# Kernel optimization log

Hardware: AMD Instinct MI355X
Metric: run time of the kernel (lower is better)

## Reference

```python
import jax, jax.numpy as jnp
import numpy as np

USER_NUM = 100000
ITEM_NUM = 100000
EMB = 128
N_USERS = 65536
N_BEH = 2097152
N_GROUPS = 2048


def setup_inputs() -> dict:
    key = jax.random.key(0)
    ks = jax.random.split(key, 7)
    user_ids = jax.random.randint(ks[0], (N_USERS,), 0, USER_NUM, dtype=jnp.int32)
    user_group_ids = jnp.sort(jax.random.randint(ks[1], (N_USERS,), 0, N_GROUPS, dtype=jnp.int32))
    behavior_item_ids = jax.random.randint(ks[2], (N_BEH,), 0, ITEM_NUM, dtype=jnp.int32)
    behavior_counts = jax.random.uniform(ks[3], (N_BEH,), dtype=jnp.float32)
    behavior_user_ids = jnp.sort(jax.random.randint(ks[4], (N_BEH,), 0, N_USERS, dtype=jnp.int32))
    user_table = jax.random.normal(ks[5], (USER_NUM, EMB), dtype=jnp.float32)
    item_table = jax.random.normal(ks[6], (ITEM_NUM, EMB), dtype=jnp.float32)
    return {
        "user_ids": user_ids,
        "user_group_ids": user_group_ids,
        "behavior_item_ids": behavior_item_ids,
        "behavior_counts": behavior_counts,
        "behavior_user_ids": behavior_user_ids,
        "user_table": user_table,
        "item_table": item_table,
        "num_groups": N_GROUPS,
    }


def reference(user_ids, user_group_ids, behavior_item_ids, behavior_counts,
              behavior_user_ids, user_table, item_table, num_groups):
    n_users = user_ids.shape[0]
    # weighted bag-of-items per user: sum_j item_emb[b_id] * count  -> [n_users, EMB]
    beh_emb = item_table[behavior_item_ids] * behavior_counts[:, None]
    per_user_beh = jax.ops.segment_sum(beh_emb, behavior_user_ids, num_segments=n_users)
    # user embedding with padding_idx=0 (id 0 -> zero vector)
    ue = user_table[user_ids] * (user_ids != 0).astype(user_table.dtype)[:, None]
    per_user = per_user_beh * ue  # personalized behavior embedding
    # pooling == 'sum' over users within each group -> [num_groups, EMB]
    group_embedding = jax.ops.segment_sum(per_user, user_group_ids, num_segments=num_groups)
    return group_embedding
```

## Files before the change

kernel.cpp:

```cpp
#include <hip/hip_runtime.h>
#include <hip/hip_fp16.h>

#define EMB 128

__global__ __launch_bounds__(256) void convert_kernel(
    const float* __restrict__ src, __half* __restrict__ dst, int n8)
{
    int t = blockIdx.x * 256 + threadIdx.x;
    if (t >= n8) return;
    const float4* s = (const float4*)src + (size_t)t * 2;
    float4 f0 = s[0];
    float4 f1 = s[1];
    union { __half h[8]; uint4 u; } pk;
    pk.h[0] = __float2half_rn(f0.x); pk.h[1] = __float2half_rn(f0.y);
    pk.h[2] = __float2half_rn(f0.z); pk.h[3] = __float2half_rn(f0.w);
    pk.h[4] = __float2half_rn(f1.x); pk.h[5] = __float2half_rn(f1.y);
    pk.h[6] = __float2half_rn(f1.z); pk.h[7] = __float2half_rn(f1.w);
    ((uint4*)dst)[t] = pk.u;
}

__global__ __launch_bounds__(256) void boundary_kernel(
    const int* __restrict__ beh_user, int* __restrict__ start,
    int n_beh, int n_users)
{
    int j = blockIdx.x * 256 + threadIdx.x;
    if (j >= n_beh) return;
    int cur  = beh_user[j];
    int prev = (j == 0) ? -1 : beh_user[j - 1];
    if (cur != prev) {
        for (int u = prev + 1; u <= cur; ++u) start[u] = j;
    }
    if (j == n_beh - 1) {
        for (int u = cur + 1; u <= n_users; ++u) start[u] = n_beh;
    }
}

__global__ __launch_bounds__(256) void per_user_kernel(
    const int*    __restrict__ user_ids,
    const int*    __restrict__ group_ids,
    const int*    __restrict__ beh_item,
    const float*  __restrict__ beh_cnt,
    const int*    __restrict__ beh_user,
    const float*  __restrict__ user_table,
    const __half* __restrict__ item_f16,
    const int*    __restrict__ start,
    float*        __restrict__ out,
    int n_users, int n_beh)
{
    const int lane = threadIdx.x & 63;
    const int half = lane >> 5;
    const int sub  = lane & 31;
    const int wave = threadIdx.x >> 6;
    const int user = blockIdx.x * 4 + wave;

    __shared__ float lds_acc[EMB];
    __shared__ int   lds_grp[4];
    if (threadIdx.x < EMB) lds_acc[threadIdx.x] = 0.0f;

    float4 acc = make_float4(0.f, 0.f, 0.f, 0.f);
    int g = -1;

    if (user < n_users) {
        int s, e;
        if (start) {
            s = start[user];
            e = start[user + 1];
        } else {
            int lo = 0, hi = n_beh;
            while (lo < hi) { int m = (lo + hi) >> 1; if (beh_user[m] < user) lo = m + 1; else hi = m; }
            s = lo;
            hi = n_beh;
            while (lo < hi) { int m = (lo + hi) >> 1; if (beh_user[m] <= user) lo = m + 1; else hi = m; }
            e = lo;
        }

        const __half* itp = item_f16 + sub * 4;

        int j = s;
        for (; j + 16 <= e; j += 16) {
            const int base = j + half * 8;
            int   bidx[8];
            float bcnt[8];
            #pragma unroll
            for (int k = 0; k < 8; ++k) { bidx[k] = beh_item[base + k]; bcnt[k] = beh_cnt[base + k]; }
            uint2 raw[8];
            #pragma unroll
            for (int k = 0; k < 8; ++k)
                raw[k] = *(const uint2*)(itp + (size_t)bidx[k] * EMB);
            #pragma unroll
            for (int k = 0; k < 8; ++k) {
                float2 f01 = __half22float2(*(const __half2*)&raw[k].x);
                float2 f23 = __half22float2(*(const __half2*)&raw[k].y);
                float  c   = bcnt[k];
                acc.x = fmaf(f01.x, c, acc.x);
                acc.y = fmaf(f01.y, c, acc.y);
                acc.z = fmaf(f23.x, c, acc.z);
                acc.w = fmaf(f23.y, c, acc.w);
            }
        }
        for (; j < e; j += 2) {
            int   jj = j + half;
            int   bi = 0;
            float c  = 0.f;
            if (jj < e) { bi = beh_item[jj]; c = beh_cnt[jj]; }
            uint2 raw = *(const uint2*)(itp + (size_t)bi * EMB);
            float2 f01 = __half22float2(*(const __half2*)&raw.x);
            float2 f23 = __half22float2(*(const __half2*)&raw.y);
            acc.x = fmaf(f01.x, c, acc.x);
            acc.y = fmaf(f01.y, c, acc.y);
            acc.z = fmaf(f23.x, c, acc.z);
            acc.w = fmaf(f23.y, c, acc.w);
        }

        acc.x += __shfl_xor(acc.x, 32, 64);
        acc.y += __shfl_xor(acc.y, 32, 64);
        acc.z += __shfl_xor(acc.z, 32, 64);
        acc.w += __shfl_xor(acc.w, 32, 64);

        int uid = user_ids[user];
        float4 ue = make_float4(0.f, 0.f, 0.f, 0.f);
        if (uid != 0) ue = *(const float4*)(user_table + (size_t)uid * EMB + sub * 4);
        acc.x *= ue.x; acc.y *= ue.y; acc.z *= ue.z; acc.w *= ue.w;

        g = group_ids[user];
    }

    const int   d0 = sub * 4 + half * 2;
    const float v0 = half ? acc.z : acc.x;
    const float v1 = half ? acc.w : acc.y;

    if (lane == 0) lds_grp[wave] = g;
    __syncthreads();

    int g0 = lds_grp[0];
    bool same = (g0 >= 0) && (lds_grp[1] == g0) && (lds_grp[2] == g0) && (lds_grp[3] == g0);
    if (same) {
        atomicAdd(&lds_acc[d0],     v0);
        atomicAdd(&lds_acc[d0 + 1], v1);
        __syncthreads();
        if (wave == 0) {
            atomicAdd(&out[(size_t)g0 * EMB + d0],     lds_acc[d0]);
            atomicAdd(&out[(size_t)g0 * EMB + d0 + 1], lds_acc[d0 + 1]);
        }
    } else if (g >= 0) {
        atomicAdd(&out[(size_t)g * EMB + d0],     v0);
        atomicAdd(&out[(size_t)g * EMB + d0 + 1], v1);
    }
}

__global__ __launch_bounds__(256) void per_user_f32_kernel(
    const int*   __restrict__ user_ids,
    const int*   __restrict__ group_ids,
    const int*   __restrict__ beh_item,
    const float* __restrict__ beh_cnt,
    const int*   __restrict__ beh_user,
    const float* __restrict__ user_table,
    const float* __restrict__ item_f32,
    float*       __restrict__ out,
    int n_users, int n_beh)
{
    const int lane = threadIdx.x & 63;
    const int wave = threadIdx.x >> 6;
    const int user = blockIdx.x * 4 + wave;
    float2 acc = make_float2(0.f, 0.f);
    int g = -1;
    if (user < n_users) {
        int lo = 0, hi = n_beh;
        while (lo < hi) { int m = (lo + hi) >> 1; if (beh_user[m] < user) lo = m + 1; else hi = m; }
        int s = lo; hi = n_beh;
        while (lo < hi) { int m = (lo + hi) >> 1; if (beh_user[m] <= user) lo = m + 1; else hi = m; }
        int e = lo;
        for (int j = s; j < e; ++j) {
            int   b = beh_item[j];
            float c = beh_cnt[j];
            float2 v = *(const float2*)(item_f32 + (size_t)b * EMB + lane * 2);
            acc.x = fmaf(v.x, c, acc.x);
            acc.y = fmaf(v.y, c, acc.y);
        }
        int uid = user_ids[user];
        float2 ue = make_float2(0.f, 0.f);
        if (uid != 0) ue = *(const float2*)(user_table + (size_t)uid * EMB + lane * 2);
        acc.x *= ue.x; acc.y *= ue.y;
        g = group_ids[user];
    }
    if (g >= 0) {
        atomicAdd(&out[(size_t)g * EMB + lane * 2],     acc.x);
        atomicAdd(&out[(size_t)g * EMB + lane * 2 + 1], acc.y);
    }
}

extern "C" void kernel_launch(void* const* d_in, const int* in_sizes, int n_in,
                              void* d_out, int out_size, void* d_ws, size_t ws_size,
                              hipStream_t stream) {
    const int*   user_ids   = (const int*)  d_in[0];
    const int*   group_ids  = (const int*)  d_in[1];
    const int*   beh_item   = (const int*)  d_in[2];
    const float* beh_cnt    = (const float*)d_in[3];
    const int*   beh_user   = (const int*)  d_in[4];
    const float* user_table = (const float*)d_in[5];
    const float* item_table = (const float*)d_in[6];

    const int n_users = in_sizes[0];
    const int n_beh   = in_sizes[2];
    const int item_n  = in_sizes[6] / EMB;

    float* out = (float*)d_out;
    hipMemsetAsync(out, 0, (size_t)out_size * sizeof(float), stream);

    size_t start_bytes = (size_t)(n_users + 1) * sizeof(int);
    size_t f16_off     = (start_bytes + 255) & ~(size_t)255;
    size_t f16_bytes   = (size_t)item_n * EMB * sizeof(__half);

    if (ws_size < f16_off + f16_bytes) {
        int ublocks = (n_users + 3) / 4;
        per_user_f32_kernel<<<ublocks, 256, 0, stream>>>(
            user_ids, group_ids, beh_item, beh_cnt, beh_user,
            user_table, item_table, out, n_users, n_beh);
        return;
    }

    int*    start    = (int*)d_ws;
    __half* item_f16 = (__half*)((char*)d_ws + f16_off);

    boundary_kernel<<<(n_beh + 255) / 256, 256, 0, stream>>>(beh_user, start, n_beh, n_users);

    int n8 = (item_n * EMB) / 8;
    convert_kernel<<<(n8 + 255) / 256, 256, 0, stream>>>(item_table, item_f16, n8);

    int ublocks = (n_users + 3) / 4;
    per_user_kernel<<<ublocks, 256, 0, stream>>>(
        user_ids, group_ids, beh_item, beh_cnt, beh_user,
        user_table, item_f16, start, out, n_users, n_beh);
}
```

Baseline: 245.0 us.

## Pack behavior item/count pairs and use 16-byte gathers with 4-way row split

The prep kernel now also writes interleaved (item id, count) int2 pairs, so the main kernel reads one 8-byte record per behavior instead of two separate arrays. The per-user kernel switches from two half-waves reading 8-byte fp16 chunks to four quarter-waves of 16 lanes each reading 16-byte chunks, reducing with two cross-lane shuffles, and has only one quarter issue the atomics. The aim is wider, fewer memory transactions per gathered row and less index traffic. In exchange it adds an extra 16 MB write plus read of the pairs buffer, more accumulator registers, and more serial atomic adds per lane.

```diff
diff --git a/kernel.cpp b/kernel.cpp
--- a/kernel.cpp
+++ b/kernel.cpp
@@ -19,12 +19,17 @@
     ((uint4*)dst)[t] = pk.u;
 }
 
-__global__ __launch_bounds__(256) void boundary_kernel(
-    const int* __restrict__ beh_user, int* __restrict__ start,
+__global__ __launch_bounds__(256) void prep_kernel(
+    const int*   __restrict__ beh_user,
+    const int*   __restrict__ beh_item,
+    const float* __restrict__ beh_cnt,
+    int*  __restrict__ start,
+    int2* __restrict__ pairs,
     int n_beh, int n_users)
 {
     int j = blockIdx.x * 256 + threadIdx.x;
     if (j >= n_beh) return;
+    pairs[j] = make_int2(beh_item[j], __float_as_int(beh_cnt[j]));
     int cur  = beh_user[j];
     int prev = (j == 0) ? -1 : beh_user[j - 1];
     if (cur != prev) {
@@ -38,18 +43,16 @@
 __global__ __launch_bounds__(256) void per_user_kernel(
     const int*    __restrict__ user_ids,
     const int*    __restrict__ group_ids,
-    const int*    __restrict__ beh_item,
-    const float*  __restrict__ beh_cnt,
-    const int*    __restrict__ beh_user,
+    const int2*   __restrict__ pairs,
     const float*  __restrict__ user_table,
     const __half* __restrict__ item_f16,
     const int*    __restrict__ start,
     float*        __restrict__ out,
-    int n_users, int n_beh)
+    int n_users)
 {
     const int lane = threadIdx.x & 63;
-    const int half = lane >> 5;
-    const int sub  = lane & 31;
+    const int q    = lane >> 4;
+    const int s16  = lane & 15;
     const int wave = threadIdx.x >> 6;
     const int user = blockIdx.x * 4 + wave;
 
@@ -57,77 +60,69 @@
     __shared__ int   lds_grp[4];
     if (threadIdx.x < EMB) lds_acc[threadIdx.x] = 0.0f;
 
-    float4 acc = make_float4(0.f, 0.f, 0.f, 0.f);
+    float acc[8] = {0.f, 0.f, 0.f, 0.f, 0.f, 0.f, 0.f, 0.f};
     int g = -1;
 
     if (user < n_users) {
-        int s, e;
-        if (start) {
-            s = start[user];
-            e = start[user + 1];
-        } else {
-            int lo = 0, hi = n_beh;
-            while (lo < hi) { int m = (lo + hi) >> 1; if (beh_user[m] < user) lo = m + 1; else hi = m; }
-            s = lo;
-            hi = n_beh;
-            while (lo < hi) { int m = (lo + hi) >> 1; if (beh_user[m] <= user) lo = m + 1; else hi = m; }
-            e = lo;
-        }
-
-        const __half* itp = item_f16 + sub * 4;
+        const int s = start[user];
+        const int e = start[user + 1];
+
+        const __half* itp = item_f16 + s16 * 8;
 
         int j = s;
         for (; j + 16 <= e; j += 16) {
-            const int base = j + half * 8;
-            int   bidx[8];
-            float bcnt[8];
-            #pragma unroll
-            for (int k = 0; k < 8; ++k) { bidx[k] = beh_item[base + k]; bcnt[k] = beh_cnt[base + k]; }
-            uint2 raw[8];
-            #pragma unroll
-            for (int k = 0; k < 8; ++k)
-                raw[k] = *(const uint2*)(itp + (size_t)bidx[k] * EMB);
-            #pragma unroll
-            for (int k = 0; k < 8; ++k) {
-                float2 f01 = __half22float2(*(const __half2*)&raw[k].x);
-                float2 f23 = __half22float2(*(const __half2*)&raw[k].y);
-                float  c   = bcnt[k];
-                acc.x = fmaf(f01.x, c, acc.x);
-                acc.y = fmaf(f01.y, c, acc.y);
-                acc.z = fmaf(f23.x, c, acc.z);
-                acc.w = fmaf(f23.y, c, acc.w);
+            int2 p[4];
+            #pragma unroll
+            for (int k = 0; k < 4; ++k) p[k] = pairs[j + q * 4 + k];
+            uint4 raw[4];
+            #pragma unroll
+            for (int k = 0; k < 4; ++k)
+                raw[k] = *(const uint4*)(itp + (size_t)p[k].x * EMB);
+            #pragma unroll
+            for (int k = 0; k < 4; ++k) {
+                float c = __int_as_float(p[k].y);
+                const __half2* h = (const __half2*)&raw[k];
+                #pragma unroll
+                for (int d = 0; d < 4; ++d) {
+                    float2 f = __half22float2(h[d]);
+                    acc[d * 2]     = fmaf(f.x, c, acc[d * 2]);
+                    acc[d * 2 + 1] = fmaf(f.y, c, acc[d * 2 + 1]);
+                }
             }
         }
-        for (; j < e; j += 2) {
-            int   jj = j + half;
-            int   bi = 0;
-            float c  = 0.f;
-            if (jj < e) { bi = beh_item[jj]; c = beh_cnt[jj]; }
-            uint2 raw = *(const uint2*)(itp + (size_t)bi * EMB);
-            float2 f01 = __half22float2(*(const __half2*)&raw.x);
-            float2 f23 = __half22float2(*(const __half2*)&raw.y);
-            acc.x = fmaf(f01.x, c, acc.x);
-            acc.y = fmaf(f01.y, c, acc.y);
-            acc.z = fmaf(f23.x, c, acc.z);
-            acc.w = fmaf(f23.y, c, acc.w);
-        }
-
-        acc.x += __shfl_xor(acc.x, 32, 64);
-        acc.y += __shfl_xor(acc.y, 32, 64);
-        acc.z += __shfl_xor(acc.z, 32, 64);
-        acc.w += __shfl_xor(acc.w, 32, 64);
+        for (; j < e; j += 4) {
+            int jj = j + q;
+            int2 p = make_int2(0, 0);
+            if (jj < e) p = pairs[jj];
+            float c = __int_as_float(p.y);
+            uint4 raw = *(const uint4*)(itp + (size_t)p.x * EMB);
+            const __half2* h = (const __half2*)&raw;
+            #pragma unroll
+            for (int d = 0; d < 4; ++d) {
+                float2 f = __half22float2(h[d]);
+                acc[d * 2]     = fmaf(f.x, c, acc[d * 2]);
+                acc[d * 2 + 1] = fmaf(f.y, c, acc[d * 2 + 1]);
+            }
+        }
+
+        #pragma unroll
+        for (int d = 0; d < 8; ++d) {
+            acc[d] += __shfl_xor(acc[d], 16, 64);
+            acc[d] += __shfl_xor(acc[d], 32, 64);
+        }
 
         int uid = user_ids[user];
-        float4 ue = make_float4(0.f, 0.f, 0.f, 0.f);
-        if (uid != 0) ue = *(const float4*)(user_table + (size_t)uid * EMB + sub * 4);
-        acc.x *= ue.x; acc.y *= ue.y; acc.z *= ue.z; acc.w *= ue.w;
+        float4 ue0 = make_float4(0.f, 0.f, 0.f, 0.f), ue1 = ue0;
+        if (uid != 0) {
+            const float* up = user_table + (size_t)uid * EMB + s16 * 8;
+            ue0 = *(const float4*)(up);
+            ue1 = *(const float4*)(up + 4);
+        }
+        acc[0] *= ue0.x; acc[1] *= ue0.y; acc[2] *= ue0.z; acc[3] *= ue0.w;
+        acc[4] *= ue1.x; acc[5] *= ue1.y; acc[6] *= ue1.z; acc[7] *= ue1.w;
 
         g = group_ids[user];
     }
-
-    const int   d0 = sub * 4 + half * 2;
-    const float v0 = half ? acc.z : acc.x;
-    const float v1 = half ? acc.w : acc.y;
 
     if (lane == 0) lds_grp[wave] = g;
     __syncthreads();
@@ -135,16 +130,19 @@
     int g0 = lds_grp[0];
     bool same = (g0 >= 0) && (lds_grp[1] == g0) && (lds_grp[2] == g0) && (lds_grp[3] == g0);
     if (same) {
-        atomicAdd(&lds_acc[d0],     v0);
-        atomicAdd(&lds_acc[d0 + 1], v1);
+        if (q == 0) {
+            #pragma unroll
+            for (int d = 0; d < 8; ++d) atomicAdd(&lds_acc[s16 * 8 + d], acc[d]);
+        }
         __syncthreads();
         if (wave == 0) {
-            atomicAdd(&out[(size_t)g0 * EMB + d0],     lds_acc[d0]);
-            atomicAdd(&out[(size_t)g0 * EMB + d0 + 1], lds_acc[d0 + 1]);
-        }
-    } else if (g >= 0) {
-        atomicAdd(&out[(size_t)g * EMB + d0],     v0);
-        atomicAdd(&out[(size_t)g * EMB + d0 + 1], v1);
+            atomicAdd(&out[(size_t)g0 * EMB + lane * 2],     lds_acc[lane * 2]);
+            atomicAdd(&out[(size_t)g0 * EMB + lane * 2 + 1], lds_acc[lane * 2 + 1]);
+        }
+    } else if (g >= 0 && q == 0) {
+        #pragma unroll
+        for (int d = 0; d < 8; ++d)
+            atomicAdd(&out[(size_t)g * EMB + s16 * 8 + d], acc[d]);
     }
 }
 
@@ -207,11 +205,13 @@
     float* out = (float*)d_out;
     hipMemsetAsync(out, 0, (size_t)out_size * sizeof(float), stream);
 
-    size_t start_bytes = (size_t)(n_users + 1) * sizeof(int);
-    size_t f16_off     = (start_bytes + 255) & ~(size_t)255;
-    size_t f16_bytes   = (size_t)item_n * EMB * sizeof(__half);
-
-    if (ws_size < f16_off + f16_bytes) {
+    size_t off = 0;
+    auto take = [&](size_t bytes) { size_t o = off; off = (off + bytes + 255) & ~(size_t)255; return o; };
+    size_t o_start = take((size_t)(n_users + 1) * sizeof(int));
+    size_t o_pairs = take((size_t)n_beh * sizeof(int2));
+    size_t o_f16   = take((size_t)item_n * EMB * sizeof(__half));
+
+    if (off > ws_size) {
         int ublocks = (n_users + 3) / 4;
         per_user_f32_kernel<<<ublocks, 256, 0, stream>>>(
             user_ids, group_ids, beh_item, beh_cnt, beh_user,
@@ -219,16 +219,17 @@
         return;
     }
 
-    int*    start    = (int*)d_ws;
-    __half* item_f16 = (__half*)((char*)d_ws + f16_off);
-
-    boundary_kernel<<<(n_beh + 255) / 256, 256, 0, stream>>>(beh_user, start, n_beh, n_users);
+    int*    start    = (int*)   ((char*)d_ws + o_start);
+    int2*   pairs    = (int2*)  ((char*)d_ws + o_pairs);
+    __half* item_f16 = (__half*)((char*)d_ws + o_f16);
+
+    prep_kernel<<<(n_beh + 255) / 256, 256, 0, stream>>>(
+        beh_user, beh_item, beh_cnt, start, pairs, n_beh, n_users);
 
     int n8 = (item_n * EMB) / 8;
     convert_kernel<<<(n8 + 255) / 256, 256, 0, stream>>>(item_table, item_f16, n8);
 
     int ublocks = (n_users + 3) / 4;
     per_user_kernel<<<ublocks, 256, 0, stream>>>(
-        user_ids, group_ids, beh_item, beh_cnt, beh_user,
-        user_table, item_f16, start, out, n_users, n_beh);
-}
+        user_ids, group_ids, pairs, user_table, item_f16, start, out, n_users);
+}
```

Measured after the change: 249.7 us. No clear change (+1.9%).
